# Kernel tuning notes

Measured on AMD Instinct MI355X. Metric: run time of the kernel, lower is better.

Reference implementation:

```python
import jax, jax.numpy as jnp
import numpy as np

D_MODEL = 1024
N_HEADS = 16
D_HEAD = D_MODEL // N_HEADS
BLOCK = 128
B, T = 2, 2048


def setup_inputs() -> dict:
    key = jax.random.key(0)
    ks = jax.random.split(key, 5)
    x = jax.random.normal(ks[0], (B, T, D_MODEL), dtype=jnp.float32)
    def init_w(k):
        # nn.Linear default init scale ~ 1/sqrt(fan_in)
        return jax.random.normal(k, (D_MODEL, D_MODEL), dtype=jnp.float32) / np.sqrt(D_MODEL).astype(np.float32)
    return {
        "x": x,
        "Wq": init_w(ks[1]),
        "Wk": init_w(ks[2]),
        "Wv": init_w(ks[3]),
        "Wo": init_w(ks[4]),
    }


def _flash_attention(Q, K, V, block_size, scale):
    """Online-softmax tiled attention over kv blocks (causal). Q,K,V: (B,H,T,d)."""
    Bb, H, Tt, d = Q.shape
    n_blocks = Tt // block_size
    # (n_blocks, B, H, block, d) so scan streams kv tiles
    Kb = K.reshape(Bb, H, n_blocks, block_size, d).transpose(2, 0, 1, 3, 4)
    Vb = V.reshape(Bb, H, n_blocks, block_size, d).transpose(2, 0, 1, 3, 4)
    starts = jnp.arange(n_blocks) * block_size
    q_pos = jnp.arange(Tt)

    def step(carry, xs):
        m, l, acc = carry
        kb, vb, st = xs
        # scores: (B,H,T,block)
        scores = scale * jnp.einsum('bhtd,bhsd->bhts', Q, kb)
        kv_pos = st + jnp.arange(block_size)
        future = kv_pos[None, :] > q_pos[:, None]          # (T, block)
        scores = jnp.where(future[None, None], -jnp.inf, scores)
        m_new = jnp.maximum(m, jnp.max(scores, axis=-1, keepdims=True))
        p = jnp.exp(scores - m_new)
        corr = jnp.exp(m - m_new)
        l = corr * l + jnp.sum(p, axis=-1, keepdims=True)
        acc = corr * acc + jnp.einsum('bhts,bhsd->bhtd', p, vb)
        return (m_new, l, acc), None

    m0 = jnp.full((Bb, H, Tt, 1), -jnp.inf, dtype=jnp.float32)
    l0 = jnp.zeros((Bb, H, Tt, 1), dtype=jnp.float32)
    a0 = jnp.zeros((Bb, H, Tt, d), dtype=jnp.float32)
    (m, l, acc), _ = jax.lax.scan(step, (m0, l0, a0), (Kb, Vb, starts))
    return acc / jnp.maximum(l, 1e-12)


def reference(x, Wq, Wk, Wv, Wo):
    Bx, Tx, _ = x.shape
    scale = 1.0 / np.sqrt(D_HEAD).astype(np.float32)
    def proj(W):  # nn.Linear: y = x @ W.T
        y = jnp.einsum('btm,nm->btn', x, W)
        return y.reshape(Bx, Tx, N_HEADS, D_HEAD).transpose(0, 2, 1, 3)
    Q, K, V = proj(Wq), proj(Wk), proj(Wv)
    O = _flash_attention(Q.astype(jnp.float32), K.astype(jnp.float32), V.astype(jnp.float32), BLOCK, scale)
    O = O.astype(x.dtype).transpose(0, 2, 1, 3).reshape(Bx, Tx, D_MODEL)
    return jnp.einsum('btm,nm->btn', O, Wo)
```

## Files before the change

### kernel.cpp

```cpp
#include <hip/hip_runtime.h>
#include <hip/hip_bf16.h>

typedef __attribute__((ext_vector_type(8))) short short8;
typedef __attribute__((ext_vector_type(4))) float f32x4;
typedef __attribute__((ext_vector_type(2))) unsigned int uint2v;
typedef __attribute__((ext_vector_type(4))) unsigned int uint4v;
typedef unsigned short u16;

#define MFMA_BF16(a, b, c) __builtin_amdgcn_mfma_f32_16x16x32_bf16(a, b, c, 0, 0, 0)

#define T_SEQ 2048
#define DMODEL 1024
#define NHEADS 16
#define DHEAD 64
#define NEG_BIG (-30000.0f)
#define QSCALE 0.1803368801111f
#define RESCALE_THR 8.0f

#if __has_builtin(__builtin_amdgcn_exp2f)
#define EXP2(x) __builtin_amdgcn_exp2f(x)
#else
#define EXP2(x) exp2f(x)
#endif

__device__ __forceinline__ unsigned bfr(unsigned u) {
  return (u + 0x7fffu + ((u >> 16) & 1u)) >> 16;
}
__device__ __forceinline__ uint4v ld8bf(const float* __restrict__ p) {
  const uint4v a = *(const uint4v*)p;
  const uint4v b = *(const uint4v*)(p + 4);
  uint4v r;
  r[0] = bfr(a[0]) | (bfr(a[1]) << 16);
  r[1] = bfr(a[2]) | (bfr(a[3]) << 16);
  r[2] = bfr(b[0]) | (bfr(b[1]) << 16);
  r[3] = bfr(b[2]) | (bfr(b[3]) << 16);
  return r;
}
__device__ __forceinline__ u16 f2bf(float f) {
  unsigned u = __float_as_uint(f);
  u += 0x7fffu + ((u >> 16) & 1u);
  return (u16)(u >> 16);
}
__device__ __forceinline__ void gld16(const u16* g, u16* l) {
  __builtin_amdgcn_global_load_lds(
      (const __attribute__((address_space(1))) unsigned int*)g,
      (__attribute__((address_space(3))) unsigned int*)l, 16, 0, 0);
}

__global__ __launch_bounds__(256) void cvt_all(
    const float* __restrict__ x, const float* __restrict__ wq,
    const float* __restrict__ wk, const float* __restrict__ wv,
    const float* __restrict__ wo, u16* __restrict__ xh, u16* __restrict__ wqh,
    u16* __restrict__ wkh, u16* __restrict__ wvh, u16* __restrict__ woh) {
  int bi = blockIdx.x;
  const float* s;
  u16* d;
  size_t base;
  if (bi < 2048) {
    s = x; d = xh; base = (size_t)bi * 2048;
  } else {
    int k = (bi - 2048) >> 9;
    int r = (bi - 2048) & 511;
    s = (k == 0) ? wq : (k == 1) ? wk : (k == 2) ? wv : wo;
    d = (k == 0) ? wqh : (k == 1) ? wkh : (k == 2) ? wvh : woh;
    base = (size_t)r * 2048;
  }
  size_t i = base + (size_t)threadIdx.x * 8;
  *(uint4v*)&d[i] = ld8bf(&s[i]);
}

__global__ __launch_bounds__(256) void gemm_qkv(
    const u16* __restrict__ X, const u16* __restrict__ Wq,
    const u16* __restrict__ Wk, const u16* __restrict__ Wv,
    u16* __restrict__ Qo, u16* __restrict__ Ko, u16* __restrict__ Vo) {
  __shared__ __attribute__((aligned(16))) u16 sm[16384];
  const int tid = threadIdx.x, lane = tid & 63, w = tid >> 6;
  const int wm = (w >> 1) * 64, wn = (w & 1) * 64;
  const int lrow = lane & 15;
  const int lk = (lane >> 4) << 3;
  const int lq = (lane >> 4) << 2;
  const int mBase = blockIdx.x * 128, nBase = blockIdx.y * 128;
  const u16* Bt = (blockIdx.z == 0) ? Wq : (blockIdx.z == 1) ? Wk : Wv;
  u16* D = (blockIdx.z == 0) ? Qo : (blockIdx.z == 1) ? Ko : Vo;
  const float scale = (blockIdx.z == 0) ? QSCALE : 1.0f;

  f32x4 acc[4][4];
#pragma unroll
  for (int mi = 0; mi < 4; mi++)
#pragma unroll
    for (int ni = 0; ni < 4; ni++) acc[mi][ni] = (f32x4)0.0f;

  auto stage = [&](int buf, int k0) {
#pragma unroll
    for (int i = 0; i < 2; i++) {
      int c = i * 256 + tid;
      int r = c >> 2, kk = (c & 3) << 3;
      gld16(&X[(size_t)(mBase + r) * 1024 + k0 + kk], &sm[buf * 4096 + c * 8]);
      gld16(&Bt[(size_t)(nBase + r) * 1024 + k0 + kk],
            &sm[8192 + buf * 4096 + c * 8]);
    }
  };

  stage(0, 0);
  __syncthreads();
  int cur = 0;
  for (int k0 = 0; k0 < 1024; k0 += 32) {
    if (k0 + 32 < 1024) stage(cur ^ 1, k0 + 32);
    short8 af[4], bf[4];
#pragma unroll
    for (int mi = 0; mi < 4; mi++)
      af[mi] = *(const short8*)&sm[cur * 4096 + (wm + mi * 16 + lrow) * 32 + lk];
#pragma unroll
    for (int ni = 0; ni < 4; ni++)
      bf[ni] =
          *(const short8*)&sm[8192 + cur * 4096 + (wn + ni * 16 + lrow) * 32 + lk];
#pragma unroll
    for (int mi = 0; mi < 4; mi++)
#pragma unroll
      for (int ni = 0; ni < 4; ni++)
        acc[mi][ni] = MFMA_BF16(af[mi], bf[ni], acc[mi][ni]);
    __syncthreads();
    cur ^= 1;
  }

  if (blockIdx.z != 2) {
#pragma unroll
    for (int mi = 0; mi < 4; mi++)
#pragma unroll
      for (int r = 0; r < 4; r++) {
        int m = mBase + wm + mi * 16 + lq + r;
        int b = m >> 11, t = m & 2047;
#pragma unroll
        for (int ni = 0; ni < 4; ni++) {
          int n = nBase + wn + ni * 16 + lrow;
          int h = n >> 6, dd = n & 63;
          D[(((size_t)(b * NHEADS + h)) * T_SEQ + t) * DHEAD + dd] =
              f2bf(acc[mi][ni][r] * scale);
        }
      }
  } else {
    u16* TT = &sm[w * 4096];
#pragma unroll
    for (int mi = 0; mi < 4; mi++)
#pragma unroll
      for (int r = 0; r < 4; r++) {
        int t_loc = mi * 16 + lq + r;
#pragma unroll
        for (int ni = 0; ni < 4; ni++) {
          int d_loc = ni * 16 + lrow;
          TT[d_loc * 64 + ((((t_loc >> 3) ^ (d_loc & 7)) << 3) | (t_loc & 7))] =
              f2bf(acc[mi][ni][r]);
        }
      }
    const int b = (mBase + wm) >> 11;
    const int t0 = (mBase + wm) & 2047;
#pragma unroll
    for (int it = 0; it < 8; it++) {
      int d_loc = it * 8 + (lane >> 3);
      int ch = lane & 7;
      short8 v = *(const short8*)&TT[d_loc * 64 + ((ch ^ (d_loc & 7)) << 3)];
      int n = nBase + wn + d_loc;
      int h = n >> 6, dd = n & 63;
      *(uint4v*)&D[(((size_t)((b * NHEADS + h) * DHEAD + dd)) * T_SEQ) + t0 +
                   ch * 8] = *(const uint4v*)&v;
    }
  }
}

__global__ __launch_bounds__(256) void attn_qt(
    const u16* __restrict__ Qg, const u16* __restrict__ Kg,
    const u16* __restrict__ Vtg, u16* __restrict__ Ob) {
  __shared__ __attribute__((aligned(16))) u16 smem[20480];

  const int tid = threadIdx.x;
  const int w = tid >> 6, lane = tid & 63;
  const int lrow = lane & 15;
  const int quad = lane >> 4;
  const int lk = quad << 3;
  const int rsw = lrow & 7;
  const int q_local = w * 16 + lrow;

  const int id = blockIdx.x;
  const int xcd = id & 7;
  const int r0 = id >> 3;
  const int rr = r0 & 31;
  const int bsub = r0 >> 5;
  const int qt = (bsub & 1) ? rr : (31 - rr);
  const int bh = xcd * 4 + bsub;
  const int b = bh >> 4, h = bh & 15;
  const int qb = qt * 64;
  const u16* Qp = Qg + (size_t)bh * T_SEQ * DHEAD;
  const u16* Kp = Kg + (size_t)bh * T_SEQ * DHEAD;
  const u16* Vp = Vtg + (size_t)bh * DHEAD * T_SEQ;

  auto stage_kv = [&](int buf, int kvb) {
#pragma unroll
    for (int i = 0; i < 2; i++) {
      int c = i * 256 + tid;
      int r = c >> 3;
      int sw = ((c & 7) ^ (r & 7)) << 3;
      gld16(&Kp[(size_t)(kvb + r) * DHEAD + sw], &smem[4096 + buf * 4096 + c * 8]);
      gld16(&Vp[(size_t)r * T_SEQ + kvb + sw], &smem[12288 + buf * 4096 + c * 8]);
    }
  };

#pragma unroll
  for (int i = 0; i < 2; i++) {
    int c = i * 256 + tid;
    int r = c >> 3, g = c & 7;
    *(uint4v*)&smem[r * 64 + ((g ^ (r & 7)) << 3)] =
        *(const uint4v*)&Qp[(size_t)(qb + r) * DHEAD + (g << 3)];
  }
  stage_kv(0, 0);
  __syncthreads();

  short8 qf[2];
#pragma unroll
  for (int ks = 0; ks < 2; ks++)
    qf[ks] = *(const short8*)&smem[q_local * 64 + ((((ks << 2) + quad) ^ rsw) << 3)];

  float mst = NEG_BIG, lst = 0.f;
  f32x4 oacc[4];
#pragma unroll
  for (int nd = 0; nd < 4; nd++) oacc[nd] = (f32x4)0.0f;

  const int ntiles = qt + 1;
  int cur = 0;
  for (int kt = 0; kt < ntiles; kt++) {
    const u16* Kc = &smem[4096 + cur * 4096];
    const u16* Vc = &smem[12288 + cur * 4096];
    if (kt + 1 < ntiles) stage_kv(cur ^ 1, (kt + 1) * 64);

    f32x4 s[4];
    __builtin_amdgcn_s_setprio(1);
#pragma unroll
    for (int kvt = 0; kvt < 4; kvt++) {
      f32x4 a = (f32x4)0.0f;
#pragma unroll
      for (int ks = 0; ks < 2; ks++) {
        short8 kf = *(const short8*)&Kc[(kvt * 16 + lrow) * 64 +
                                        ((((ks << 2) + quad) ^ rsw) << 3)];
        a = MFMA_BF16(kf, qf[ks], a);
      }
      s[kvt] = a;
    }
    __builtin_amdgcn_s_setprio(0);

    if (kt == qt) {
#pragma unroll
      for (int kvt = 0; kvt < 4; kvt++)
#pragma unroll
        for (int r = 0; r < 4; r++)
          if (kvt * 16 + quad * 4 + r > q_local) s[kvt][r] = NEG_BIG;
    }

    float mx = NEG_BIG;
#pragma unroll
    for (int kvt = 0; kvt < 4; kvt++)
      mx = fmaxf(mx, fmaxf(fmaxf(s[kvt][0], s[kvt][1]),
                           fmaxf(s[kvt][2], s[kvt][3])));
    mx = fmaxf(mx, __shfl_xor(mx, 16));
    mx = fmaxf(mx, __shfl_xor(mx, 32));
    if (!__all(mx <= mst + RESCALE_THR)) {
      float mn = fmaxf(mst, mx);
      float corr = EXP2(mst - mn);
      mst = mn;
      lst *= corr;
#pragma unroll
      for (int nd = 0; nd < 4; nd++) oacc[nd] *= corr;
    }
    float ls = 0.f;
#pragma unroll
    for (int kvt = 0; kvt < 4; kvt++)
#pragma unroll
      for (int r = 0; r < 4; r++) {
        float pv = EXP2(s[kvt][r] - mst);
        s[kvt][r] = pv;
        ls += pv;
      }
    ls += __shfl_xor(ls, 16);
    ls += __shfl_xor(ls, 32);
    lst += ls;

#pragma unroll
    for (int kvt = 0; kvt < 4; kvt++) {
      uint2v pk;
      pk[0] = (__float_as_uint(s[kvt][0]) >> 16) |
              (__float_as_uint(s[kvt][1]) & 0xffff0000u);
      pk[1] = (__float_as_uint(s[kvt][2]) >> 16) |
              (__float_as_uint(s[kvt][3]) & 0xffff0000u);
      *(uint2v*)&smem[q_local * 64 +
                      ((((kvt << 1) | (quad >> 1)) ^ rsw) << 3) +
                      ((quad & 1) << 2)] = pk;
    }

    __builtin_amdgcn_s_setprio(1);
#pragma unroll
    for (int ks = 0; ks < 2; ks++) {
      short8 pf = *(const short8*)&smem[q_local * 64 +
                                        ((((ks << 2) + quad) ^ rsw) << 3)];
#pragma unroll
      for (int nd = 0; nd < 4; nd++) {
        short8 vf = *(const short8*)&Vc[(nd * 16 + lrow) * 64 +
                                        ((((ks << 2) + quad) ^ rsw) << 3)];
        oacc[nd] = MFMA_BF16(vf, pf, oacc[nd]);
      }
    }
    __builtin_amdgcn_s_setprio(0);

    __syncthreads();
    cur ^= 1;
  }

  float inv = 1.f / lst;
  size_t rowbase = ((size_t)(b * T_SEQ + qb + q_local)) * DMODEL + h * DHEAD;
#pragma unroll
  for (int nd = 0; nd < 4; nd++) {
    uint2v pk;
    pk[0] = (unsigned)f2bf(oacc[nd][0] * inv) |
            ((unsigned)f2bf(oacc[nd][1] * inv) << 16);
    pk[1] = (unsigned)f2bf(oacc[nd][2] * inv) |
            ((unsigned)f2bf(oacc[nd][3] * inv) << 16);
    *(uint2v*)&Ob[rowbase + nd * 16 + quad * 4] = pk;
  }
}

__global__ __launch_bounds__(256) void gemm_out_bf(const u16* __restrict__ O,
                                                   const u16* __restrict__ Wo,
                                                   float* __restrict__ Out) {
  __shared__ __attribute__((aligned(16))) u16 As[2][128 * 32];
  __shared__ __attribute__((aligned(16))) u16 Bs[2][64 * 32];
  const int tid = threadIdx.x, lane = tid & 63, w = tid >> 6;
  const int wm = (w >> 1) * 64, wn = (w & 1) * 32;
  const int lrow = lane & 15;
  const int lk = (lane >> 4) << 3;
  const int lq = (lane >> 4) << 2;
  const int mBase = blockIdx.x * 128, nBase = blockIdx.y * 64;

  f32x4 acc[4][2];
#pragma unroll
  for (int mi = 0; mi < 4; mi++)
#pragma unroll
    for (int ni = 0; ni < 2; ni++) acc[mi][ni] = (f32x4)0.0f;

  auto stage = [&](int buf, int k0) {
#pragma unroll
    for (int i = 0; i < 2; i++) {
      int c = i * 256 + tid;
      int r = c >> 2, kk = (c & 3) << 3;
      gld16(&O[(size_t)(mBase + r) * 1024 + k0 + kk], &As[buf][c * 8]);
    }
    int r = tid >> 2, kk = (tid & 3) << 3;
    gld16(&Wo[(size_t)(nBase + r) * 1024 + k0 + kk], &Bs[buf][tid * 8]);
  };

  stage(0, 0);
  __syncthreads();
  int cur = 0;
  for (int k0 = 0; k0 < 1024; k0 += 32) {
    if (k0 + 32 < 1024) stage(cur ^ 1, k0 + 32);
    short8 af[4], bf[2];
#pragma unroll
    for (int mi = 0; mi < 4; mi++)
      af[mi] = *(const short8*)&As[cur][(wm + mi * 16 + lrow) * 32 + lk];
#pragma unroll
    for (int ni = 0; ni < 2; ni++)
      bf[ni] = *(const short8*)&Bs[cur][(wn + ni * 16 + lrow) * 32 + lk];
#pragma unroll
    for (int mi = 0; mi < 4; mi++)
#pragma unroll
      for (int ni = 0; ni < 2; ni++)
        acc[mi][ni] = MFMA_BF16(af[mi], bf[ni], acc[mi][ni]);
    __syncthreads();
    cur ^= 1;
  }
#pragma unroll
  for (int mi = 0; mi < 4; mi++)
#pragma unroll
    for (int r = 0; r < 4; r++) {
      int m = mBase + wm + mi * 16 + lq + r;
#pragma unroll
      for (int ni = 0; ni < 2; ni++)
        Out[(size_t)m * DMODEL + nBase + wn + ni * 16 + lrow] = acc[mi][ni][r];
    }
}

extern "C" void kernel_launch(void* const* d_in, const int* in_sizes, int n_in,
                              void* d_out, int out_size, void* d_ws,
                              size_t ws_size, hipStream_t stream) {
  const float* x = (const float*)d_in[0];
  const float* Wq = (const float*)d_in[1];
  const float* Wk = (const float*)d_in[2];
  const float* Wv = (const float*)d_in[3];
  const float* Wo = (const float*)d_in[4];
  float* out = (float*)d_out;

  u16* xh = (u16*)d_ws;
  u16* wqh = xh + 4194304;
  u16* wkh = wqh + 1048576;
  u16* wvh = wkh + 1048576;
  u16* woh = wvh + 1048576;
  u16* Q = woh + 1048576;
  u16* K = Q + 4194304;
  u16* V = K + 4194304;
  u16* O = V + 4194304;

  cvt_all<<<dim3(4096), 256, 0, stream>>>(x, Wq, Wk, Wv, Wo, xh, wqh, wkh, wvh, woh);
  gemm_qkv<<<dim3(32, 8, 3), 256, 0, stream>>>(xh, wqh, wkh, wvh, Q, K, V);
  attn_qt<<<dim3(1024), 256, 0, stream>>>(Q, K, V, O);
  gemm_out_bf<<<dim3(32, 16), 256, 0, stream>>>(O, woh, out);
}
```

Before: 178.2 us.

## Split KV tiles across two wave groups in attention and remap GEMM blocks per XCD

The attention kernel now runs 512 threads per block as two 4-wave groups. Each group processes alternating KV tiles for the same 64-query tile, keeping its own online-softmax state, and the two partial results are merged through shared memory at the end. The aim is to halve the serial KV loop length per block and add latency hiding, at the cost of double the LDS footprint, a final merge step and lower occupancy. The GEMM launches are flattened to 1D with an XCD-aware mapping so that neighbouring M tiles share an XCD's L2, and Q fragments are now loaded directly from global memory.

```diff
diff --git a/kernel.cpp b/kernel.cpp
--- a/kernel.cpp
+++ b/kernel.cpp
@@ -79,10 +79,16 @@
   const int lrow = lane & 15;
   const int lk = (lane >> 4) << 3;
   const int lq = (lane >> 4) << 2;
-  const int mBase = blockIdx.x * 128, nBase = blockIdx.y * 128;
-  const u16* Bt = (blockIdx.z == 0) ? Wq : (blockIdx.z == 1) ? Wk : Wv;
-  u16* D = (blockIdx.z == 0) ? Qo : (blockIdx.z == 1) ? Ko : Vo;
-  const float scale = (blockIdx.z == 0) ? QSCALE : 1.0f;
+
+  const int id = blockIdx.x;
+  const int xcd = id & 7, r8 = id >> 3;
+  const int xo = r8 & 3, yz = r8 >> 2;
+  const int y = yz & 7, z = yz >> 3;
+  const int mBase = (xcd * 4 + xo) * 128, nBase = y * 128;
+
+  const u16* Bt = (z == 0) ? Wq : (z == 1) ? Wk : Wv;
+  u16* D = (z == 0) ? Qo : (z == 1) ? Ko : Vo;
+  const float scale = (z == 0) ? QSCALE : 1.0f;
 
   f32x4 acc[4][4];
 #pragma unroll
@@ -123,7 +129,7 @@
     cur ^= 1;
   }
 
-  if (blockIdx.z != 2) {
+  if (z != 2) {
 #pragma unroll
     for (int mi = 0; mi < 4; mi++)
 #pragma unroll
@@ -167,161 +173,177 @@
   }
 }
 
-__global__ __launch_bounds__(256) void attn_qt(
+__global__ __launch_bounds__(512) void attn_kvsplit(
     const u16* __restrict__ Qg, const u16* __restrict__ Kg,
     const u16* __restrict__ Vtg, u16* __restrict__ Ob) {
-  __shared__ __attribute__((aligned(16))) u16 smem[20480];
+  __shared__ __attribute__((aligned(16))) u16 smem[40960];
 
   const int tid = threadIdx.x;
   const int w = tid >> 6, lane = tid & 63;
+  const int g = w >> 2;
+  const int wg = w & 3;
   const int lrow = lane & 15;
   const int quad = lane >> 4;
   const int lk = quad << 3;
   const int rsw = lrow & 7;
-  const int q_local = w * 16 + lrow;
+  const int q_local = wg * 16 + lrow;
 
   const int id = blockIdx.x;
   const int xcd = id & 7;
   const int r0 = id >> 3;
-  const int rr = r0 & 31;
-  const int bsub = r0 >> 5;
-  const int qt = (bsub & 1) ? rr : (31 - rr);
-  const int bh = xcd * 4 + bsub;
+  const int qt = 31 - (r0 >> 2);
+  const int bh = xcd * 4 + (r0 & 3);
   const int b = bh >> 4, h = bh & 15;
   const int qb = qt * 64;
   const u16* Qp = Qg + (size_t)bh * T_SEQ * DHEAD;
   const u16* Kp = Kg + (size_t)bh * T_SEQ * DHEAD;
   const u16* Vp = Vtg + (size_t)bh * DHEAD * T_SEQ;
 
-  auto stage_kv = [&](int buf, int kvb) {
-#pragma unroll
-    for (int i = 0; i < 2; i++) {
-      int c = i * 256 + tid;
-      int r = c >> 3;
-      int sw = ((c & 7) ^ (r & 7)) << 3;
-      gld16(&Kp[(size_t)(kvb + r) * DHEAD + sw], &smem[4096 + buf * 4096 + c * 8]);
-      gld16(&Vp[(size_t)r * T_SEQ + kvb + sw], &smem[12288 + buf * 4096 + c * 8]);
-    }
+  auto stage_tile = [&](int T, int p) {
+    if (T > qt) return;
+    const int slot = (p << 1) | (T & 1);
+    const int c = tid;
+    const int r = c >> 3;
+    const int sw = ((c & 7) ^ (r & 7)) << 3;
+    gld16(&Kp[(size_t)(T * 64 + r) * DHEAD + sw],
+          &smem[8192 + slot * 4096 + c * 8]);
+    gld16(&Vp[(size_t)r * T_SEQ + T * 64 + sw],
+          &smem[24576 + slot * 4096 + c * 8]);
   };
 
-#pragma unroll
-  for (int i = 0; i < 2; i++) {
-    int c = i * 256 + tid;
-    int r = c >> 3, g = c & 7;
-    *(uint4v*)&smem[r * 64 + ((g ^ (r & 7)) << 3)] =
-        *(const uint4v*)&Qp[(size_t)(qb + r) * DHEAD + (g << 3)];
-  }
-  stage_kv(0, 0);
-  __syncthreads();
+  stage_tile(0, 0);
+  stage_tile(1, 0);
 
   short8 qf[2];
 #pragma unroll
   for (int ks = 0; ks < 2; ks++)
-    qf[ks] = *(const short8*)&smem[q_local * 64 + ((((ks << 2) + quad) ^ rsw) << 3)];
+    qf[ks] = *(const short8*)&Qp[(size_t)(qb + q_local) * DHEAD + ks * 32 + lk];
 
   float mst = NEG_BIG, lst = 0.f;
   f32x4 oacc[4];
 #pragma unroll
   for (int nd = 0; nd < 4; nd++) oacc[nd] = (f32x4)0.0f;
-
-  const int ntiles = qt + 1;
-  int cur = 0;
-  for (int kt = 0; kt < ntiles; kt++) {
-    const u16* Kc = &smem[4096 + cur * 4096];
-    const u16* Vc = &smem[12288 + cur * 4096];
-    if (kt + 1 < ntiles) stage_kv(cur ^ 1, (kt + 1) * 64);
-
-    f32x4 s[4];
-    __builtin_amdgcn_s_setprio(1);
-#pragma unroll
-    for (int kvt = 0; kvt < 4; kvt++) {
-      f32x4 a = (f32x4)0.0f;
+  __syncthreads();
+
+  const int Smax = (qt + 2) >> 1;
+  for (int s = 0; s < Smax; s++) {
+    const int p = s & 1;
+    stage_tile(2 * s + 2, p ^ 1);
+    stage_tile(2 * s + 3, p ^ 1);
+    const int myt = 2 * s + g;
+    if (myt <= qt) {
+      const u16* Kc = &smem[8192 + ((p << 1) | g) * 4096];
+      const u16* Vc = &smem[24576 + ((p << 1) | g) * 4096];
+
+      f32x4 sv[4];
+      __builtin_amdgcn_s_setprio(1);
+#pragma unroll
+      for (int kvt = 0; kvt < 4; kvt++) {
+        f32x4 a = (f32x4)0.0f;
+#pragma unroll
+        for (int ks = 0; ks < 2; ks++) {
+          short8 kf = *(const short8*)&Kc[(kvt * 16 + lrow) * 64 +
+                                          ((((ks << 2) + quad) ^ rsw) << 3)];
+          a = MFMA_BF16(kf, qf[ks], a);
+        }
+        sv[kvt] = a;
+      }
+      __builtin_amdgcn_s_setprio(0);
+
+      if (myt == qt) {
+#pragma unroll
+        for (int kvt = 0; kvt < 4; kvt++)
+#pragma unroll
+          for (int r = 0; r < 4; r++)
+            if (kvt * 16 + quad * 4 + r > q_local) sv[kvt][r] = NEG_BIG;
+      }
+
+      float mx = NEG_BIG;
+#pragma unroll
+      for (int kvt = 0; kvt < 4; kvt++)
+        mx = fmaxf(mx, fmaxf(fmaxf(sv[kvt][0], sv[kvt][1]),
+                             fmaxf(sv[kvt][2], sv[kvt][3])));
+      mx = fmaxf(mx, __shfl_xor(mx, 16));
+      mx = fmaxf(mx, __shfl_xor(mx, 32));
+      if (!__all(mx <= mst + RESCALE_THR)) {
+        float mn = fmaxf(mst, mx);
+        float corr = EXP2(mst - mn);
+        mst = mn;
+        lst *= corr;
+#pragma unroll
+        for (int nd = 0; nd < 4; nd++) oacc[nd] *= corr;
+      }
+      float ls = 0.f;
+#pragma unroll
+      for (int kvt = 0; kvt < 4; kvt++)
+#pragma unroll
+        for (int r = 0; r < 4; r++) {
+          float pv = EXP2(sv[kvt][r] - mst);
+          sv[kvt][r] = pv;
+          ls += pv;
+        }
+      ls += __shfl_xor(ls, 16);
+      ls += __shfl_xor(ls, 32);
+      lst += ls;
+
+#pragma unroll
+      for (int kvt = 0; kvt < 4; kvt++) {
+        uint2v pk;
+        pk[0] = (__float_as_uint(sv[kvt][0]) >> 16) |
+                (__float_as_uint(sv[kvt][1]) & 0xffff0000u);
+        pk[1] = (__float_as_uint(sv[kvt][2]) >> 16) |
+                (__float_as_uint(sv[kvt][3]) & 0xffff0000u);
+        *(uint2v*)&smem[g * 4096 + q_local * 64 +
+                        ((((kvt << 1) | (quad >> 1)) ^ rsw) << 3) +
+                        ((quad & 1) << 2)] = pk;
+      }
+
+      __builtin_amdgcn_s_setprio(1);
 #pragma unroll
       for (int ks = 0; ks < 2; ks++) {
-        short8 kf = *(const short8*)&Kc[(kvt * 16 + lrow) * 64 +
-                                        ((((ks << 2) + quad) ^ rsw) << 3)];
-        a = MFMA_BF16(kf, qf[ks], a);
-      }
-      s[kvt] = a;
-    }
-    __builtin_amdgcn_s_setprio(0);
-
-    if (kt == qt) {
-#pragma unroll
-      for (int kvt = 0; kvt < 4; kvt++)
-#pragma unroll
-        for (int r = 0; r < 4; r++)
-          if (kvt * 16 + quad * 4 + r > q_local) s[kvt][r] = NEG_BIG;
-    }
-
-    float mx = NEG_BIG;
-#pragma unroll
-    for (int kvt = 0; kvt < 4; kvt++)
-      mx = fmaxf(mx, fmaxf(fmaxf(s[kvt][0], s[kvt][1]),
-                           fmaxf(s[kvt][2], s[kvt][3])));
-    mx = fmaxf(mx, __shfl_xor(mx, 16));
-    mx = fmaxf(mx, __shfl_xor(mx, 32));
-    if (!__all(mx <= mst + RESCALE_THR)) {
-      float mn = fmaxf(mst, mx);
-      float corr = EXP2(mst - mn);
-      mst = mn;
-      lst *= corr;
-#pragma unroll
-      for (int nd = 0; nd < 4; nd++) oacc[nd] *= corr;
-    }
-    float ls = 0.f;
-#pragma unroll
-    for (int kvt = 0; kvt < 4; kvt++)
-#pragma unroll
-      for (int r = 0; r < 4; r++) {
-        float pv = EXP2(s[kvt][r] - mst);
-        s[kvt][r] = pv;
-        ls += pv;
-      }
-    ls += __shfl_xor(ls, 16);
-    ls += __shfl_xor(ls, 32);
-    lst += ls;
-
-#pragma unroll
-    for (int kvt = 0; kvt < 4; kvt++) {
+        short8 pf = *(const short8*)&smem[g * 4096 + q_local * 64 +
+                                          ((((ks << 2) + quad) ^ rsw) << 3)];
+#pragma unroll
+        for (int nd = 0; nd < 4; nd++) {
+          short8 vf = *(const short8*)&Vc[(nd * 16 + lrow) * 64 +
+                                          ((((ks << 2) + quad) ^ rsw) << 3)];
+          oacc[nd] = MFMA_BF16(vf, pf, oacc[nd]);
+        }
+      }
+      __builtin_amdgcn_s_setprio(0);
+    }
+    __syncthreads();
+  }
+
+  float* O1 = (float*)&smem[8192];
+  float* ml = (float*)&smem[24576];
+  if (g == 1) {
+#pragma unroll
+    for (int nd = 0; nd < 4; nd++)
+      *(f32x4*)&O1[q_local * 64 + ((((nd << 2) | quad) ^ rsw) << 2)] = oacc[nd];
+    if (quad == 0) {
+      ml[q_local] = mst;
+      ml[64 + q_local] = lst;
+    }
+  }
+  __syncthreads();
+  if (g == 0) {
+    const float m1 = ml[q_local], l1 = ml[64 + q_local];
+    const float M = fmaxf(mst, m1);
+    const float c0 = EXP2(mst - M), c1 = EXP2(m1 - M);
+    const float inv = 1.f / (c0 * lst + c1 * l1);
+    size_t rowbase = ((size_t)(b * T_SEQ + qb + q_local)) * DMODEL + h * DHEAD;
+#pragma unroll
+    for (int nd = 0; nd < 4; nd++) {
+      f32x4 o1 = *(const f32x4*)&O1[q_local * 64 +
+                                    ((((nd << 2) | quad) ^ rsw) << 2)];
       uint2v pk;
-      pk[0] = (__float_as_uint(s[kvt][0]) >> 16) |
-              (__float_as_uint(s[kvt][1]) & 0xffff0000u);
-      pk[1] = (__float_as_uint(s[kvt][2]) >> 16) |
-              (__float_as_uint(s[kvt][3]) & 0xffff0000u);
-      *(uint2v*)&smem[q_local * 64 +
-                      ((((kvt << 1) | (quad >> 1)) ^ rsw) << 3) +
-                      ((quad & 1) << 2)] = pk;
-    }
-
-    __builtin_amdgcn_s_setprio(1);
-#pragma unroll
-    for (int ks = 0; ks < 2; ks++) {
-      short8 pf = *(const short8*)&smem[q_local * 64 +
-                                        ((((ks << 2) + quad) ^ rsw) << 3)];
-#pragma unroll
-      for (int nd = 0; nd < 4; nd++) {
-        short8 vf = *(const short8*)&Vc[(nd * 16 + lrow) * 64 +
-                                        ((((ks << 2) + quad) ^ rsw) << 3)];
-        oacc[nd] = MFMA_BF16(vf, pf, oacc[nd]);
-      }
-    }
-    __builtin_amdgcn_s_setprio(0);
-
-    __syncthreads();
-    cur ^= 1;
-  }
-
-  float inv = 1.f / lst;
-  size_t rowbase = ((size_t)(b * T_SEQ + qb + q_local)) * DMODEL + h * DHEAD;
-#pragma unroll
-  for (int nd = 0; nd < 4; nd++) {
-    uint2v pk;
-    pk[0] = (unsigned)f2bf(oacc[nd][0] * inv) |
-            ((unsigned)f2bf(oacc[nd][1] * inv) << 16);
-    pk[1] = (unsigned)f2bf(oacc[nd][2] * inv) |
-            ((unsigned)f2bf(oacc[nd][3] * inv) << 16);
-    *(uint2v*)&Ob[rowbase + nd * 16 + quad * 4] = pk;
+      pk[0] = (unsigned)f2bf((c0 * oacc[nd][0] + c1 * o1[0]) * inv) |
+              ((unsigned)f2bf((c0 * oacc[nd][1] + c1 * o1[1]) * inv) << 16);
+      pk[1] = (unsigned)f2bf((c0 * oacc[nd][2] + c1 * o1[2]) * inv) |
+              ((unsigned)f2bf((c0 * oacc[nd][3] + c1 * o1[3]) * inv) << 16);
+      *(uint2v*)&Ob[rowbase + nd * 16 + quad * 4] = pk;
+    }
   }
 }
 
@@ -335,7 +357,11 @@
   const int lrow = lane & 15;
   const int lk = (lane >> 4) << 3;
   const int lq = (lane >> 4) << 2;
-  const int mBase = blockIdx.x * 128, nBase = blockIdx.y * 64;
+
+  const int id = blockIdx.x;
+  const int xcd = id & 7, r8 = id >> 3;
+  const int xo = r8 & 3, y = r8 >> 2;
+  const int mBase = (xcd * 4 + xo) * 128, nBase = y * 64;
 
   f32x4 acc[4][2];
 #pragma unroll
@@ -406,7 +432,7 @@
   u16* O = V + 4194304;
 
   cvt_all<<<dim3(4096), 256, 0, stream>>>(x, Wq, Wk, Wv, Wo, xh, wqh, wkh, wvh, woh);
-  gemm_qkv<<<dim3(32, 8, 3), 256, 0, stream>>>(xh, wqh, wkh, wvh, Q, K, V);
-  attn_qt<<<dim3(1024), 256, 0, stream>>>(Q, K, V, O);
-  gemm_out_bf<<<dim3(32, 16), 256, 0, stream>>>(O, woh, out);
-}
+  gemm_qkv<<<dim3(768), 256, 0, stream>>>(xh, wqh, wkh, wvh, Q, K, V);
+  attn_kvsplit<<<dim3(1024), 512, 0, stream>>>(Q, K, V, O);
+  gemm_out_bf<<<dim3(512), 256, 0, stream>>>(O, woh, out);
+}
```

New measurement: 175.1 us. No clear change (-1.7%).
